# Kernel tuning notes

Measured on AMD Instinct MI355X. Metric: run time of the kernel, lower is better.

The kernel has to match this reference:

```python
import jax, jax.numpy as jnp
import numpy as np

T, B, INPUT_DIM, HIDDEN_DIM = 256, 128, 512, 512
N_QUBITS = HIDDEN_DIM  # must match hidden_dim for the gate elementwise math


def _qlayer(v, theta):
    # Closed-form of the PennyLane circuit: RX(x_i)RX(theta_i) per wire, CNOT
    # ladder, <Z_k>.  <Z_k> = prod_{j<=k} cos(v_j + theta_j).
    return jnp.cumprod(jnp.cos(v + theta), axis=-1)


def setup_inputs() -> dict:
    key = jax.random.key(0)
    ks = jax.random.split(key, 13)
    comb = INPUT_DIM + HIDDEN_DIM
    s = 1.0 / np.sqrt(comb)
    inp = {"inputs": jax.random.normal(ks[0], (T, B, INPUT_DIM), dtype=jnp.float32)}
    names = ["forget", "input", "update", "output"]
    for n, i in zip(names, range(4)):
        inp[f"W_{n}"] = jax.random.uniform(ks[1 + 3 * i], (HIDDEN_DIM, comb), jnp.float32, -s, s)
        inp[f"b_{n}"] = jax.random.uniform(ks[2 + 3 * i], (HIDDEN_DIM,), jnp.float32, -s, s)
        inp[f"theta_{n}"] = jax.random.normal(ks[3 + 3 * i], (N_QUBITS,), dtype=jnp.float32)
    return inp


def reference(inputs, W_forget, b_forget, theta_forget,
              W_input, b_input, theta_input,
              W_update, b_update, theta_update,
              W_output, b_output, theta_output):
    Bsz = inputs.shape[1]
    h0 = jnp.zeros((Bsz, HIDDEN_DIM), dtype=inputs.dtype)
    c0 = jnp.zeros((Bsz, HIDDEN_DIM), dtype=inputs.dtype)

    def step(carry, x):
        hx, cx = carry
        comb = jnp.concatenate([x, hx], axis=1)  # [B, input+hidden]
        f = jax.nn.sigmoid(_qlayer(comb @ W_forget.T + b_forget, theta_forget))
        i = jax.nn.sigmoid(_qlayer(comb @ W_input.T + b_input, theta_input))
        g = jnp.tanh(_qlayer(comb @ W_update.T + b_update, theta_update))
        o = jax.nn.sigmoid(_qlayer(comb @ W_output.T + b_output, theta_output))
        cx = f * cx + i * g
        hx = o * jnp.tanh(cx)
        return (hx, cx), hx

    (hx, cx), outputs = jax.lax.scan(step, (h0, c0), inputs)
    return outputs, (hx, cx)
```

## Files before the change

kernel.cpp:

```cpp
#include <hip/hip_runtime.h>
#include <hip/hip_bf16.h>

#define T_STEPS 256
#define BATCH   128
#define DIN     512
#define DH      512
#define NGATE   2048
#define NCL     8
#define WPC     32
#define ROWS_CL 16
#define NWG     (NCL * WPC)

typedef __attribute__((ext_vector_type(8))) short short8;
typedef __attribute__((ext_vector_type(4))) float f32x4;
typedef unsigned long long u64;

#define OUT_HX ((size_t)T_STEPS * BATCH * DH)
#define OUT_CX (OUT_HX + (size_t)BATCH * DH)

#define WB_OFF    0
#define XB_OFF    (4 * 1024 * 1024)
#define BT_OFF    (XB_OFF + 32 * 1024 * 1024)
#define CL_OFF    (BT_OFF + 8192)
#define CL_STRIDE (160 * 1024)
#define CLV_OFF   0
#define CLH_OFF   131072
#define CLF_OFF   147456
#define CLFB_OFF  (CLF_OFF + 4096)
#define SLOT_STRIDE 32
#define BOOT_OFF  (CL_OFF + NCL * CL_STRIDE)

#define LDS_W_BYTES 131072
#define LDS_TOTAL   (LDS_W_BYTES + 4 * DH * 4)

__device__ inline ushort f2bf(float x) {
  uint u = __float_as_uint(x);
  u += 0x7fffu + ((u >> 16) & 1u);
  return (ushort)(u >> 16);
}
__device__ inline float sigm(float x) { return 1.f / (1.f + __expf(-x)); }
__device__ inline float tanhf_(float x) { return 1.f - 2.f / (1.f + __expf(2.f * x)); }

__device__ inline u64 ald64(const u64* p) {
  return __hip_atomic_load(p, __ATOMIC_RELAXED, __HIP_MEMORY_SCOPE_AGENT);
}
__device__ inline void ast32(uint* p, uint v) {
  __hip_atomic_store(p, v, __ATOMIC_RELAXED, __HIP_MEMORY_SCOPE_AGENT);
}
__device__ inline int aldi(const int* p) {
  return __hip_atomic_load(p, __ATOMIC_RELAXED, __HIP_MEMORY_SCOPE_AGENT);
}
__device__ inline void asti(int* p, int v) {
  __hip_atomic_store(p, v, __ATOMIC_RELAXED, __HIP_MEMORY_SCOPE_AGENT);
}
__device__ inline void l1inv() {
  asm volatile("buffer_inv" ::: "memory");
  asm volatile("s_waitcnt vmcnt(0)" ::: "memory");
}

union U16 { u64 q[2]; short8 s; };
union UF2 { u64 q; float f[2]; };

__global__ void k_prep_w(const float* __restrict__ Wf, const float* __restrict__ Wi,
                         const float* __restrict__ Wu, const float* __restrict__ Wo,
                         ushort* __restrict__ Wb) {
  size_t i4 = ((size_t)blockIdx.x * 256 + threadIdx.x) * 4;
  if (i4 >= (size_t)NGATE * 1024) return;
  int row = (int)(i4 >> 10);
  int col = (int)(i4 & 1023);
  const float* W = (row < 512) ? Wf : (row < 1024) ? Wi : (row < 1536) ? Wu : Wo;
  int r = row & 511;
  float4 w = *(const float4*)&W[(size_t)r * 1024 + col];
  ushort4 o = make_ushort4(f2bf(w.x), f2bf(w.y), f2bf(w.z), f2bf(w.w));
  *(ushort4*)&Wb[i4] = o;
}

__global__ void k_prep_x(const float* __restrict__ X, ushort* __restrict__ Xb) {
  size_t i4 = ((size_t)blockIdx.x * 256 + threadIdx.x) * 4;
  if (i4 >= (size_t)T_STEPS * BATCH * DIN) return;
  float4 xv = *(const float4*)&X[i4];
  ushort4 o = make_ushort4(f2bf(xv.x), f2bf(xv.y), f2bf(xv.z), f2bf(xv.w));
  *(ushort4*)&Xb[i4] = o;
}

__global__ void k_prep_misc(const float* __restrict__ bf_, const float* __restrict__ tf_,
                            const float* __restrict__ bi_, const float* __restrict__ ti_,
                            const float* __restrict__ bu_, const float* __restrict__ tu_,
                            const float* __restrict__ bo_, const float* __restrict__ to_,
                            float* __restrict__ bt, char* __restrict__ clbase,
                            int* __restrict__ boot) {
  int idx = blockIdx.x * 256 + threadIdx.x;
  if (idx < NGATE) {
    int g = idx >> 9, k = idx & 511;
    const float* b = (g == 0) ? bf_ : (g == 1) ? bi_ : (g == 2) ? bu_ : bo_;
    const float* t = (g == 0) ? tf_ : (g == 1) ? ti_ : (g == 2) ? tu_ : to_;
    bt[idx] = b[k] + t[k];
  }
  if (idx < NCL * 4096) {
    int c = idx >> 12, w = idx & 4095;
    ((uint*)(clbase + (size_t)c * CL_STRIDE + CLH_OFF))[w] = 0u;
  }
  if (idx < NCL * 2048) {
    int c = idx >> 11, w = idx & 2047;
    ((int*)(clbase + (size_t)c * CL_STRIDE + CLF_OFF))[w] = 0;
  }
  if (idx < 16) boot[idx] = 0;
}

template<bool L>
__device__ __forceinline__ void run_main(
    const ushort* __restrict__ Xb, const ushort* __restrict__ Wb,
    const float* __restrict__ bt, char* cl, float* __restrict__ out,
    int cluster, int mem, ushort* wlds, float* lds_g) {
  const int tid  = threadIdx.x;
  const int lane = tid & 63;
  const int wave = tid >> 6;

  float*  v_cl  = (float*)(cl + CLV_OFF);
  u64*    h_cl  = (u64*)(cl + CLH_OFF);
  uint*   h_cl32= (uint*)(cl + CLH_OFF);
  int*    slotA = (int*)(cl + CLF_OFF);
  int*    slotB = (int*)(cl + CLFB_OFF);

  const int nb    = mem * 64 + wave * 16;
  const int ar    = lane & 15;
  const int kx    = (lane >> 4) << 3;
  const int crow0 = cluster * ROWS_CL;
  const int row   = crow0 + mem;
  const int wrow  = wave * 16 + ar;

  {
    const char* wsrc = (const char*)(Wb + (size_t)(mem * 64) * 1024);
#pragma unroll
    for (int it = 0; it < 32; ++it) {
      int idx16 = it * 256 + tid;
      int r  = idx16 >> 7;
      int kb = (idx16 & 127) << 4;
      short8 w = *(const short8*)(wsrc + (size_t)r * 2048 + kb);
      *(short8*)((char*)wlds + (size_t)r * 2048 + (kb ^ ((r & 7) << 4))) = w;
    }
  }
#define WFRAG(KT) (*(const short8*)((const char*)wlds + (size_t)wrow * 2048 + \
                    ((((KT) * 64) + (kx << 1)) ^ ((ar & 7) << 4))))

  float btr[8];
  {
    const int e0 = lane << 3;
#pragma unroll
    for (int j = 0; j < 8; ++j) btr[j] = bt[wave * DH + e0 + j];
  }
  __syncthreads();

  float c0 = 0.f, c1 = 0.f;
  f32x4 accE = {0.f, 0.f, 0.f, 0.f}, accO = {0.f, 0.f, 0.f, 0.f};

#define XPART(TT) do {                                                        \
    accE = (f32x4){0.f, 0.f, 0.f, 0.f};                                       \
    accO = (f32x4){0.f, 0.f, 0.f, 0.f};                                       \
    const ushort* Ax = Xb + ((size_t)(TT) * BATCH + crow0 + ar) * DIN + kx;   \
    _Pragma("unroll")                                                         \
    for (int kt = 0; kt < 16; kt += 2) {                                      \
      short8 a0 = *(const short8*)(Ax + kt * 32);                             \
      short8 a1 = *(const short8*)(Ax + (kt + 1) * 32);                       \
      accE = __builtin_amdgcn_mfma_f32_16x16x32_bf16(a0, WFRAG(kt), accE, 0, 0, 0);     \
      accO = __builtin_amdgcn_mfma_f32_16x16x32_bf16(a1, WFRAG(kt + 1), accO, 0, 0, 0); \
    }                                                                         \
  } while (0)

  XPART(0);

  for (int t = 0; t < T_STEPS; ++t) {
    const int ep = t + 1;
    {
      U16 af[16];
#pragma unroll
      for (int kt = 0; kt < 16; ++kt) {
        const u64* p = h_cl + (((size_t)ar * DH + kt * 32 + kx) >> 2);
        if constexpr (L) { af[kt].q[0] = p[0];       af[kt].q[1] = p[1]; }
        else             { af[kt].q[0] = ald64(p);   af[kt].q[1] = ald64(p + 1); }
      }
#pragma unroll
      for (int kt = 0; kt < 16; kt += 2) {
        accE = __builtin_amdgcn_mfma_f32_16x16x32_bf16(af[kt].s,     WFRAG(16 + kt),     accE, 0, 0, 0);
        accO = __builtin_amdgcn_mfma_f32_16x16x32_bf16(af[kt + 1].s, WFRAG(16 + kt + 1), accO, 0, 0, 0);
      }
    }
    {
      const int rbase = (lane >> 4) << 2;
      float* vp = v_cl + (size_t)rbase * NGATE + nb + ar;
#pragma unroll
      for (int r = 0; r < 4; ++r) {
        float val = accE[r] + accO[r];
        if constexpr (L) vp[(size_t)r * NGATE] = val;
        else             ast32((uint*)&vp[(size_t)r * NGATE], __float_as_uint(val));
      }
    }
    __syncthreads();
    if (tid == 0) asti(&slotA[mem * SLOT_STRIDE], ep);

    if (mem < ROWS_CL) {
      if (wave == 0) {
        for (;;) {
          int s = (lane < WPC) ? aldi(&slotA[lane * SLOT_STRIDE]) : ep;
          if (__all(s >= ep)) break;
          __builtin_amdgcn_s_sleep(1);
        }
        if constexpr (L) l1inv();
      }
      __syncthreads();
      asm volatile("" ::: "memory");
      {
        const int g  = wave;
        const int e0 = lane << 3;
        const u64* vr = (const u64*)(v_cl + (size_t)mem * NGATE + g * DH + e0);
        UF2 w0, w1, w2, w3;
        if constexpr (L) { w0.q = vr[0]; w1.q = vr[1]; w2.q = vr[2]; w3.q = vr[3]; }
        else { w0.q = ald64(vr); w1.q = ald64(vr + 1); w2.q = ald64(vr + 2); w3.q = ald64(vr + 3); }
        float p0 = __cosf(w0.f[0] + btr[0]);
        float p1 = __cosf(w0.f[1] + btr[1]);
        float p2 = __cosf(w1.f[0] + btr[2]);
        float p3 = __cosf(w1.f[1] + btr[3]);
        float p4 = __cosf(w2.f[0] + btr[4]);
        float p5 = __cosf(w2.f[1] + btr[5]);
        float p6 = __cosf(w3.f[0] + btr[6]);
        float p7 = __cosf(w3.f[1] + btr[7]);
        float q0 = p0, q1 = q0 * p1, q2 = q1 * p2, q3 = q2 * p3;
        float q4 = q3 * p4, q5 = q4 * p5, q6 = q5 * p6, q7 = q6 * p7;
        float a = q7;
#pragma unroll
        for (int off = 1; off < 64; off <<= 1) {
          float o = __shfl_up(a, off);
          a = (lane >= off) ? a * o : a;
        }
        float ex = __shfl_up(a, 1);
        ex = (lane == 0) ? 1.f : ex;
        float G0 = ex * q0, G1 = ex * q1, G2 = ex * q2, G3 = ex * q3;
        float G4 = ex * q4, G5 = ex * q5, G6 = ex * q6, G7 = ex * q7;
        float4 r0, r1;
        if (g == 2) {
          r0 = make_float4(tanhf_(G0), tanhf_(G1), tanhf_(G2), tanhf_(G3));
          r1 = make_float4(tanhf_(G4), tanhf_(G5), tanhf_(G6), tanhf_(G7));
        } else {
          r0 = make_float4(sigm(G0), sigm(G1), sigm(G2), sigm(G3));
          r1 = make_float4(sigm(G4), sigm(G5), sigm(G6), sigm(G7));
        }
        *(float4*)&lds_g[g * DH + e0]     = r0;
        *(float4*)&lds_g[g * DH + e0 + 4] = r1;
      }
      __syncthreads();
      {
        const int k = tid << 1;
        float f0 = lds_g[0 * DH + k], f1 = lds_g[0 * DH + k + 1];
        float i0 = lds_g[1 * DH + k], i1 = lds_g[1 * DH + k + 1];
        float u0 = lds_g[2 * DH + k], u1 = lds_g[2 * DH + k + 1];
        float o0 = lds_g[3 * DH + k], o1 = lds_g[3 * DH + k + 1];
        c0 = f0 * c0 + i0 * u0;
        c1 = f1 * c1 + i1 * u1;
        float h0 = o0 * tanhf_(c0);
        float h1 = o1 * tanhf_(c1);
        float2 hp = make_float2(h0, h1);
        *(float2*)&out[((size_t)t * BATCH + row) * DH + k] = hp;
        uint hbits = ((uint)f2bf(h1) << 16) | (uint)f2bf(h0);
        if constexpr (L) h_cl32[mem * 256 + tid] = hbits;
        else             ast32(&h_cl32[mem * 256 + tid], hbits);
        if (t == T_STEPS - 1) {
          *(float2*)&out[OUT_HX + (size_t)row * DH + k] = hp;
          float2 cp = make_float2(c0, c1);
          *(float2*)&out[OUT_CX + (size_t)row * DH + k] = cp;
        }
      }
      __syncthreads();
      if (tid == 0) asti(&slotB[mem * SLOT_STRIDE], ep);
    }

    if (t + 1 < T_STEPS) {
      XPART(t + 1);
      if (wave == 0) {
        for (;;) {
          int s = (lane < ROWS_CL) ? aldi(&slotB[lane * SLOT_STRIDE]) : ep;
          if (__all(s >= ep)) break;
          __builtin_amdgcn_s_sleep(1);
        }
        if constexpr (L) l1inv();
      }
      __syncthreads();
      asm volatile("" ::: "memory");
    }
  }
#undef XPART
#undef WFRAG
}

__global__ __launch_bounds__(256, 1) void qlstm_main(
    const ushort* __restrict__ Xb, const ushort* __restrict__ Wb,
    const float* __restrict__ bt, char* __restrict__ clbase,
    int* __restrict__ boot, float* __restrict__ out) {
  extern __shared__ char smem[];
  ushort* wlds  = (ushort*)smem;
  float*  lds_g = (float*)(smem + LDS_W_BYTES);

  __shared__ int shboot[4];
  const int tid = threadIdx.x;

  if (tid == 0) {
    uint xcc;
    asm volatile("s_getreg_b32 %0, hwreg(HW_REG_XCC_ID)" : "=s"(xcc));
    xcc &= 7;
    int slot = __hip_atomic_fetch_add(&boot[xcc], 1, __ATOMIC_RELAXED, __HIP_MEMORY_SCOPE_AGENT);
    __hip_atomic_fetch_add(&boot[8], 1, __ATOMIC_RELAXED, __HIP_MEMORY_SCOPE_AGENT);
    while (__hip_atomic_load(&boot[8], __ATOMIC_RELAXED, __HIP_MEMORY_SCOPE_AGENT) < NWG)
      __builtin_amdgcn_s_sleep(8);
    int ok = 1;
#pragma unroll
    for (int c2 = 0; c2 < NCL; ++c2)
      ok &= (__hip_atomic_load(&boot[c2], __ATOMIC_RELAXED, __HIP_MEMORY_SCOPE_AGENT) == WPC);
    shboot[0] = (int)xcc;
    shboot[1] = slot;
    shboot[2] = ok;
  }
  __syncthreads();
  const int local_ok = shboot[2];
  const int cluster  = local_ok ? shboot[0] : ((int)blockIdx.x & 7);
  const int mem      = local_ok ? shboot[1] : ((int)blockIdx.x >> 3);
  char* cl = clbase + (size_t)cluster * CL_STRIDE;

  if (local_ok)
    run_main<true>(Xb, Wb, bt, cl, out, cluster, mem, wlds, lds_g);
  else
    run_main<false>(Xb, Wb, bt, cl, out, cluster, mem, wlds, lds_g);
}

extern "C" void kernel_launch(void* const* d_in, const int* in_sizes, int n_in,
                              void* d_out, int out_size, void* d_ws, size_t ws_size,
                              hipStream_t stream) {
  const float* X  = (const float*)d_in[0];
  const float* Wf = (const float*)d_in[1];
  const float* bf = (const float*)d_in[2];
  const float* tf = (const float*)d_in[3];
  const float* Wi = (const float*)d_in[4];
  const float* bi = (const float*)d_in[5];
  const float* ti = (const float*)d_in[6];
  const float* Wu = (const float*)d_in[7];
  const float* bu = (const float*)d_in[8];
  const float* tu = (const float*)d_in[9];
  const float* Wo = (const float*)d_in[10];
  const float* bo = (const float*)d_in[11];
  const float* to = (const float*)d_in[12];

  char* ws = (char*)d_ws;
  ushort* Wb     = (ushort*)(ws + WB_OFF);
  ushort* Xb     = (ushort*)(ws + XB_OFF);
  float*  bt     = (float*)(ws + BT_OFF);
  char*   clbase = ws + CL_OFF;
  int*    boot   = (int*)(ws + BOOT_OFF);
  float*  out    = (float*)d_out;

  static bool attr_set = false;
  if (!attr_set) {
    hipFuncSetAttribute((const void*)qlstm_main,
                        hipFuncAttributeMaxDynamicSharedMemorySize, LDS_TOTAL);
    attr_set = true;
  }

  k_prep_w<<<dim3((NGATE * 1024 / 4 + 255) / 256), dim3(256), 0, stream>>>(Wf, Wi, Wu, Wo, Wb);
  k_prep_x<<<dim3((T_STEPS * BATCH * DIN / 4 + 255) / 256), dim3(256), 0, stream>>>(X, Xb);
  k_prep_misc<<<dim3(256), dim3(256), 0, stream>>>(bf, tf, bi, ti, bu, tu, bo, to, bt, clbase, boot);
  qlstm_main<<<dim3(NWG), dim3(256), LDS_TOTAL, stream>>>(Xb, Wb, bt, clbase, boot, out);
}
```

Baseline: 1.628 ms.

## Halve workgroups per cluster, keep only recurrent weights in LDS, stream input weights

Each cluster now uses 16 workgroups instead of 32. Each workgroup computes 128 gate columns with two accumulator sets and also handles one batch row's gate nonlinearity and cell update, so the barrier set shrinks and no workgroup sits idle. Only the hidden-part weights stay in LDS. The input-projection weights are now read from global memory on every step inside XPART. This cuts synchronisation participants and the number of resident workgroups, at the cost of twice the MFMA work per workgroup and extra global weight traffic in the input projection.

Result: slower. 2.914 ms (+79.0%).

```diff
diff --git a/kernel.cpp b/kernel.cpp
--- a/kernel.cpp
+++ b/kernel.cpp
@@ -7,7 +7,7 @@
 #define DH      512
 #define NGATE   2048
 #define NCL     8
-#define WPC     32
+#define WPC     16
 #define ROWS_CL 16
 #define NWG     (NCL * WPC)
 
@@ -122,26 +122,27 @@
   int*    slotA = (int*)(cl + CLF_OFF);
   int*    slotB = (int*)(cl + CLFB_OFF);
 
-  const int nb    = mem * 64 + wave * 16;
+  const int nb    = mem * 128 + wave * 32;
   const int ar    = lane & 15;
   const int kx    = (lane >> 4) << 3;
   const int crow0 = cluster * ROWS_CL;
   const int row   = crow0 + mem;
-  const int wrow  = wave * 16 + ar;
+  const int cl0   = wave * 32 + ar;
+  const int cl1   = cl0 + 16;
 
   {
-    const char* wsrc = (const char*)(Wb + (size_t)(mem * 64) * 1024);
 #pragma unroll
     for (int it = 0; it < 32; ++it) {
       int idx16 = it * 256 + tid;
-      int r  = idx16 >> 7;
-      int kb = (idx16 & 127) << 4;
-      short8 w = *(const short8*)(wsrc + (size_t)r * 2048 + kb);
-      *(short8*)((char*)wlds + (size_t)r * 2048 + (kb ^ ((r & 7) << 4))) = w;
-    }
-  }
-#define WFRAG(KT) (*(const short8*)((const char*)wlds + (size_t)wrow * 2048 + \
-                    ((((KT) * 64) + (kx << 1)) ^ ((ar & 7) << 4))))
+      int c  = idx16 >> 6;
+      int kb = (idx16 & 63) << 4;
+      const char* src = (const char*)(Wb + (size_t)(mem * 128 + c) * 1024 + 512) + kb;
+      short8 w = *(const short8*)src;
+      *(short8*)((char*)wlds + (size_t)c * 1024 + (kb ^ ((c & 7) << 4))) = w;
+    }
+  }
+#define WHFRAG(CL, KT) (*(const short8*)((const char*)wlds + (size_t)(CL) * 1024 + \
+                        ((((KT) * 64) + (kx << 1)) ^ (((CL) & 7) << 4))))
 
   float btr[8];
   {
@@ -152,18 +153,26 @@
   __syncthreads();
 
   float c0 = 0.f, c1 = 0.f;
-  f32x4 accE = {0.f, 0.f, 0.f, 0.f}, accO = {0.f, 0.f, 0.f, 0.f};
+  f32x4 accE0 = {0,0,0,0}, accO0 = {0,0,0,0}, accE1 = {0,0,0,0}, accO1 = {0,0,0,0};
 
 #define XPART(TT) do {                                                        \
-    accE = (f32x4){0.f, 0.f, 0.f, 0.f};                                       \
-    accO = (f32x4){0.f, 0.f, 0.f, 0.f};                                       \
-    const ushort* Ax = Xb + ((size_t)(TT) * BATCH + crow0 + ar) * DIN + kx;   \
+    accE0 = (f32x4){0,0,0,0}; accO0 = (f32x4){0,0,0,0};                       \
+    accE1 = (f32x4){0,0,0,0}; accO1 = (f32x4){0,0,0,0};                       \
+    const ushort* Ax  = Xb + ((size_t)(TT) * BATCH + crow0 + ar) * DIN + kx;  \
+    const ushort* Bx0 = Wb + (size_t)(mem * 128 + cl0) * 1024 + kx;           \
+    const ushort* Bx1 = Wb + (size_t)(mem * 128 + cl1) * 1024 + kx;           \
     _Pragma("unroll")                                                         \
     for (int kt = 0; kt < 16; kt += 2) {                                      \
-      short8 a0 = *(const short8*)(Ax + kt * 32);                             \
-      short8 a1 = *(const short8*)(Ax + (kt + 1) * 32);                       \
-      accE = __builtin_amdgcn_mfma_f32_16x16x32_bf16(a0, WFRAG(kt), accE, 0, 0, 0);     \
-      accO = __builtin_amdgcn_mfma_f32_16x16x32_bf16(a1, WFRAG(kt + 1), accO, 0, 0, 0); \
+      short8 a0  = *(const short8*)(Ax  + kt * 32);                           \
+      short8 a1  = *(const short8*)(Ax  + (kt + 1) * 32);                     \
+      short8 b00 = *(const short8*)(Bx0 + kt * 32);                           \
+      short8 b01 = *(const short8*)(Bx0 + (kt + 1) * 32);                     \
+      short8 b10 = *(const short8*)(Bx1 + kt * 32);                           \
+      short8 b11 = *(const short8*)(Bx1 + (kt + 1) * 32);                     \
+      accE0 = __builtin_amdgcn_mfma_f32_16x16x32_bf16(a0, b00, accE0, 0, 0, 0); \
+      accE1 = __builtin_amdgcn_mfma_f32_16x16x32_bf16(a0, b10, accE1, 0, 0, 0); \
+      accO0 = __builtin_amdgcn_mfma_f32_16x16x32_bf16(a1, b01, accO0, 0, 0, 0); \
+      accO1 = __builtin_amdgcn_mfma_f32_16x16x32_bf16(a1, b11, accO1, 0, 0, 0); \
     }                                                                         \
   } while (0)
 
@@ -181,8 +190,10 @@
       }
 #pragma unroll
       for (int kt = 0; kt < 16; kt += 2) {
-        accE = __builtin_amdgcn_mfma_f32_16x16x32_bf16(af[kt].s,     WFRAG(16 + kt),     accE, 0, 0, 0);
-        accO = __builtin_amdgcn_mfma_f32_16x16x32_bf16(af[kt + 1].s, WFRAG(16 + kt + 1), accO, 0, 0, 0);
+        accE0 = __builtin_amdgcn_mfma_f32_16x16x32_bf16(af[kt].s,     WHFRAG(cl0, kt),     accE0, 0, 0, 0);
+        accE1 = __builtin_amdgcn_mfma_f32_16x16x32_bf16(af[kt].s,     WHFRAG(cl1, kt),     accE1, 0, 0, 0);
+        accO0 = __builtin_amdgcn_mfma_f32_16x16x32_bf16(af[kt + 1].s, WHFRAG(cl0, kt + 1), accO0, 0, 0, 0);
+        accO1 = __builtin_amdgcn_mfma_f32_16x16x32_bf16(af[kt + 1].s, WHFRAG(cl1, kt + 1), accO1, 0, 0, 0);
       }
     }
     {
@@ -190,18 +201,99 @@
       float* vp = v_cl + (size_t)rbase * NGATE + nb + ar;
 #pragma unroll
       for (int r = 0; r < 4; ++r) {
-        float val = accE[r] + accO[r];
-        if constexpr (L) vp[(size_t)r * NGATE] = val;
-        else             ast32((uint*)&vp[(size_t)r * NGATE], __float_as_uint(val));
+        float v0 = accE0[r] + accO0[r];
+        float v1 = accE1[r] + accO1[r];
+        if constexpr (L) {
+          vp[(size_t)r * NGATE]      = v0;
+          vp[(size_t)r * NGATE + 16] = v1;
+        } else {
+          ast32((uint*)&vp[(size_t)r * NGATE],      __float_as_uint(v0));
+          ast32((uint*)&vp[(size_t)r * NGATE + 16], __float_as_uint(v1));
+        }
       }
     }
     __syncthreads();
     if (tid == 0) asti(&slotA[mem * SLOT_STRIDE], ep);
 
-    if (mem < ROWS_CL) {
+    if (wave == 0) {
+      for (;;) {
+        int s = (lane < WPC) ? aldi(&slotA[lane * SLOT_STRIDE]) : ep;
+        if (__all(s >= ep)) break;
+        __builtin_amdgcn_s_sleep(1);
+      }
+      if constexpr (L) l1inv();
+    }
+    __syncthreads();
+    asm volatile("" ::: "memory");
+
+    {
+      const int g  = wave;
+      const int e0 = lane << 3;
+      const u64* vr = (const u64*)(v_cl + (size_t)mem * NGATE + g * DH + e0);
+      UF2 w0, w1, w2, w3;
+      if constexpr (L) { w0.q = vr[0]; w1.q = vr[1]; w2.q = vr[2]; w3.q = vr[3]; }
+      else { w0.q = ald64(vr); w1.q = ald64(vr + 1); w2.q = ald64(vr + 2); w3.q = ald64(vr + 3); }
+      float p0 = __cosf(w0.f[0] + btr[0]);
+      float p1 = __cosf(w0.f[1] + btr[1]);
+      float p2 = __cosf(w1.f[0] + btr[2]);
+      float p3 = __cosf(w1.f[1] + btr[3]);
+      float p4 = __cosf(w2.f[0] + btr[4]);
+      float p5 = __cosf(w2.f[1] + btr[5]);
+      float p6 = __cosf(w3.f[0] + btr[6]);
+      float p7 = __cosf(w3.f[1] + btr[7]);
+      float q0 = p0, q1 = q0 * p1, q2 = q1 * p2, q3 = q2 * p3;
+      float q4 = q3 * p4, q5 = q4 * p5, q6 = q5 * p6, q7 = q6 * p7;
+      float a = q7;
+#pragma unroll
+      for (int off = 1; off < 64; off <<= 1) {
+        float o = __shfl_up(a, off);
+        a = (lane >= off) ? a * o : a;
+      }
+      float ex = __shfl_up(a, 1);
+      ex = (lane == 0) ? 1.f : ex;
+      float G0 = ex * q0, G1 = ex * q1, G2 = ex * q2, G3 = ex * q3;
+      float G4 = ex * q4, G5 = ex * q5, G6 = ex * q6, G7 = ex * q7;
+      float4 r0, r1;
+      if (g == 2) {
+        r0 = make_float4(tanhf_(G0), tanhf_(G1), tanhf_(G2), tanhf_(G3));
+        r1 = make_float4(tanhf_(G4), tanhf_(G5), tanhf_(G6), tanhf_(G7));
+      } else {
+        r0 = make_float4(sigm(G0), sigm(G1), sigm(G2), sigm(G3));
+        r1 = make_float4(sigm(G4), sigm(G5), sigm(G6), sigm(G7));
+      }
+      *(float4*)&lds_g[g * DH + e0]     = r0;
+      *(float4*)&lds_g[g * DH + e0 + 4] = r1;
+    }
+    __syncthreads();
+    {
+      const int k = tid << 1;
+      float f0 = lds_g[0 * DH + k], f1 = lds_g[0 * DH + k + 1];
+      float i0 = lds_g[1 * DH + k], i1 = lds_g[1 * DH + k + 1];
+      float u0 = lds_g[2 * DH + k], u1 = lds_g[2 * DH + k + 1];
+      float o0 = lds_g[3 * DH + k], o1 = lds_g[3 * DH + k + 1];
+      c0 = f0 * c0 + i0 * u0;
+      c1 = f1 * c1 + i1 * u1;
+      float h0 = o0 * tanhf_(c0);
+      float h1 = o1 * tanhf_(c1);
+      float2 hp = make_float2(h0, h1);
+      *(float2*)&out[((size_t)t * BATCH + row) * DH + k] = hp;
+      uint hbits = ((uint)f2bf(h1) << 16) | (uint)f2bf(h0);
+      if constexpr (L) h_cl32[mem * 256 + tid] = hbits;
+      else             ast32(&h_cl32[mem * 256 + tid], hbits);
+      if (t == T_STEPS - 1) {
+        *(float2*)&out[OUT_HX + (size_t)row * DH + k] = hp;
+        float2 cp = make_float2(c0, c1);
+        *(float2*)&out[OUT_CX + (size_t)row * DH + k] = cp;
+      }
+    }
+    __syncthreads();
+    if (tid == 0) asti(&slotB[mem * SLOT_STRIDE], ep);
+
+    if (t + 1 < T_STEPS) {
+      XPART(t + 1);
       if (wave == 0) {
         for (;;) {
-          int s = (lane < WPC) ? aldi(&slotA[lane * SLOT_STRIDE]) : ep;
+          int s = (lane < WPC) ? aldi(&slotB[lane * SLOT_STRIDE]) : ep;
           if (__all(s >= ep)) break;
           __builtin_amdgcn_s_sleep(1);
         }
@@ -209,86 +301,10 @@
       }
       __syncthreads();
       asm volatile("" ::: "memory");
-      {
-        const int g  = wave;
-        const int e0 = lane << 3;
-        const u64* vr = (const u64*)(v_cl + (size_t)mem * NGATE + g * DH + e0);
-        UF2 w0, w1, w2, w3;
-        if constexpr (L) { w0.q = vr[0]; w1.q = vr[1]; w2.q = vr[2]; w3.q = vr[3]; }
-        else { w0.q = ald64(vr); w1.q = ald64(vr + 1); w2.q = ald64(vr + 2); w3.q = ald64(vr + 3); }
-        float p0 = __cosf(w0.f[0] + btr[0]);
-        float p1 = __cosf(w0.f[1] + btr[1]);
-        float p2 = __cosf(w1.f[0] + btr[2]);
-        float p3 = __cosf(w1.f[1] + btr[3]);
-        float p4 = __cosf(w2.f[0] + btr[4]);
-        float p5 = __cosf(w2.f[1] + btr[5]);
-        float p6 = __cosf(w3.f[0] + btr[6]);
-        float p7 = __cosf(w3.f[1] + btr[7]);
-        float q0 = p0, q1 = q0 * p1, q2 = q1 * p2, q3 = q2 * p3;
-        float q4 = q3 * p4, q5 = q4 * p5, q6 = q5 * p6, q7 = q6 * p7;
-        float a = q7;
-#pragma unroll
-        for (int off = 1; off < 64; off <<= 1) {
-          float o = __shfl_up(a, off);
-          a = (lane >= off) ? a * o : a;
-        }
-        float ex = __shfl_up(a, 1);
-        ex = (lane == 0) ? 1.f : ex;
-        float G0 = ex * q0, G1 = ex * q1, G2 = ex * q2, G3 = ex * q3;
-        float G4 = ex * q4, G5 = ex * q5, G6 = ex * q6, G7 = ex * q7;
-        float4 r0, r1;
-        if (g == 2) {
-          r0 = make_float4(tanhf_(G0), tanhf_(G1), tanhf_(G2), tanhf_(G3));
-          r1 = make_float4(tanhf_(G4), tanhf_(G5), tanhf_(G6), tanhf_(G7));
-        } else {
-          r0 = make_float4(sigm(G0), sigm(G1), sigm(G2), sigm(G3));
-          r1 = make_float4(sigm(G4), sigm(G5), sigm(G6), sigm(G7));
-        }
-        *(float4*)&lds_g[g * DH + e0]     = r0;
-        *(float4*)&lds_g[g * DH + e0 + 4] = r1;
-      }
-      __syncthreads();
-      {
-        const int k = tid << 1;
-        float f0 = lds_g[0 * DH + k], f1 = lds_g[0 * DH + k + 1];
-        float i0 = lds_g[1 * DH + k], i1 = lds_g[1 * DH + k + 1];
-        float u0 = lds_g[2 * DH + k], u1 = lds_g[2 * DH + k + 1];
-        float o0 = lds_g[3 * DH + k], o1 = lds_g[3 * DH + k + 1];
-        c0 = f0 * c0 + i0 * u0;
-        c1 = f1 * c1 + i1 * u1;
-        float h0 = o0 * tanhf_(c0);
-        float h1 = o1 * tanhf_(c1);
-        float2 hp = make_float2(h0, h1);
-        *(float2*)&out[((size_t)t * BATCH + row) * DH + k] = hp;
-        uint hbits = ((uint)f2bf(h1) << 16) | (uint)f2bf(h0);
-        if constexpr (L) h_cl32[mem * 256 + tid] = hbits;
-        else             ast32(&h_cl32[mem * 256 + tid], hbits);
-        if (t == T_STEPS - 1) {
-          *(float2*)&out[OUT_HX + (size_t)row * DH + k] = hp;
-          float2 cp = make_float2(c0, c1);
-          *(float2*)&out[OUT_CX + (size_t)row * DH + k] = cp;
-        }
-      }
-      __syncthreads();
-      if (tid == 0) asti(&slotB[mem * SLOT_STRIDE], ep);
-    }
-
-    if (t + 1 < T_STEPS) {
-      XPART(t + 1);
-      if (wave == 0) {
-        for (;;) {
-          int s = (lane < ROWS_CL) ? aldi(&slotB[lane * SLOT_STRIDE]) : ep;
-          if (__all(s >= ep)) break;
-          __builtin_amdgcn_s_sleep(1);
-        }
-        if constexpr (L) l1inv();
-      }
-      __syncthreads();
-      asm volatile("" ::: "memory");
     }
   }
 #undef XPART
-#undef WFRAG
+#undef WHFRAG
 }
 
 __global__ __launch_bounds__(256, 1) void qlstm_main(
```
